# Optimization experiments

Hardware: AMD Instinct MI355X
Metric: run time of the kernel (lower is better)

The kernel has to match this reference:

```python
import jax, jax.numpy as jnp
import numpy as np

T, B, S = 32, 64, 64          # tgt_len, batch, src_len
V, E, H, L = 32000, 512, 1024, 2  # vocab, word_vec, rnn_size, layers


def setup_inputs() -> dict:
    key = jax.random.key(0)
    ks = jax.random.split(key, 16)
    s = 0.02
    emb = jax.random.normal(ks[5], (V, E)) * s
    emb = emb.at[0].set(0.0)  # padding_idx=0 row is zero
    return {
        "input": jax.random.randint(ks[0], (T, B), 0, V),
        "h0": jax.random.normal(ks[1], (L, B, H)) * s,
        "c0": jax.random.normal(ks[2], (L, B, H)) * s,
        "context": jax.random.normal(ks[3], (S, B, H)),
        "init_output": jax.random.normal(ks[4], (B, H)) * s,
        "embedding": emb,
        "W_ih0": jax.random.normal(ks[6], (4 * H, E + H)) * s,  # layer0 input = emb + input-feed
        "W_hh0": jax.random.normal(ks[7], (4 * H, H)) * s,
        "b0": jnp.zeros((4 * H,), jnp.float32),
        "W_ih1": jax.random.normal(ks[8], (4 * H, H)) * s,
        "W_hh1": jax.random.normal(ks[9], (4 * H, H)) * s,
        "b1": jnp.zeros((4 * H,), jnp.float32),
        "attn_in_w": jax.random.normal(ks[10], (H, H)) * s,
        "attn_out_w": jax.random.normal(ks[11], (H, 2 * H)) * s,
        "copy_in_w": jax.random.normal(ks[12], (H, H)) * s,
    }


def _lstm_cell(x, h, c, W_ih, W_hh, b):
    g = x @ W_ih.T + h @ W_hh.T + b
    i, f, gg, o = jnp.split(g, 4, axis=-1)  # PyTorch gate order i,f,g,o
    c_new = jax.nn.sigmoid(f) * c + jax.nn.sigmoid(i) * jnp.tanh(gg)
    h_new = jax.nn.sigmoid(o) * jnp.tanh(c_new)
    return h_new, c_new


def _global_attention(in_w, out_w, query, ctx):
    # query: (B,H), ctx: (B,S,H)
    q = query @ in_w.T
    scores = jnp.einsum('bd,bsd->bs', q, ctx)
    a = jax.nn.softmax(scores, axis=-1)
    wctx = jnp.einsum('bs,bsd->bd', a, ctx)
    out = jnp.tanh(jnp.concatenate([wctx, query], axis=-1) @ out_w.T)
    return out, a


def reference(input, h0, c0, context, init_output, embedding,
              W_ih0, W_hh0, b0, W_ih1, W_hh1, b1,
              attn_in_w, attn_out_w, copy_in_w):
    ctx = jnp.transpose(context, (1, 0, 2))  # (B,S,H)
    emb = embedding[input]                    # (T,B,E)

    def step(carry, emb_t):
        h, c, out_feed = carry
        x = jnp.concatenate([emb_t, out_feed], axis=-1)  # input feed
        h0n, c0n = _lstm_cell(x, h[0], c[0], W_ih0, W_hh0, b0)
        h1n, c1n = _lstm_cell(h0n, h[1], c[1], W_ih1, W_hh1, b1)
        out, a_std = _global_attention(attn_in_w, attn_out_w, h1n, ctx)
        # copy attention: only the weights are kept by the original module
        qc = out @ copy_in_w.T
        a_copy = jax.nn.softmax(jnp.einsum('bd,bsd->bs', qc, ctx), axis=-1)
        new_carry = (jnp.stack([h0n, h1n]), jnp.stack([c0n, c1n]), out)
        return new_carry, (out, a_std, a_copy)

    (h_T, c_T, _), (outputs, attn_std, attn_copy) = jax.lax.scan(
        step, (h0, c0, init_output), emb)
    return outputs, (h_T, c_T), attn_std, attn_copy
```

## Files before the change

kernel.cpp:

```cpp
#include <hip/hip_runtime.h>

typedef unsigned short u16;
typedef unsigned int   u32;
typedef __attribute__((ext_vector_type(8))) __bf16 bfrag;
typedef __attribute__((ext_vector_type(4))) float  f32x4;
typedef __attribute__((ext_vector_type(2))) u32    u32x2;
typedef __attribute__((ext_vector_type(4))) u32    u32x4;

#define DEVI static __device__ __forceinline__

#define ST2SC(p, v)    asm volatile("global_store_short %0, %1, off sc0 sc1"   :: "v"(p), "v"(v) : "memory")
#define ST4SC(p, v)    asm volatile("global_store_dword %0, %1, off sc0 sc1"   :: "v"(p), "v"(v) : "memory")
#define ST8SC(p, v)    asm volatile("global_store_dwordx2 %0, %1, off sc0 sc1" :: "v"(p), "v"(v) : "memory")
#define ST16SC(p, v)   asm volatile("global_store_dwordx4 %0, %1, off sc0 sc1" :: "v"(p), "v"(v) : "memory")
#define VMFLUSH()      asm volatile("s_waitcnt vmcnt(0)" ::: "memory")

constexpr long OUT_OFF = 0;
constexpr long HT_OFF  = 2097152;
constexpr long CT_OFF  = 2228224;
constexpr long AS_OFF  = 2359296;
constexpr long AC_OFF  = 2490368;

constexpr long WAO_O   = 0;
constexpr long CTX_O   = 4194304;
constexpr long OFR_O   = 0;
constexpr long H0R_O   = 4194304;
constexpr long H1R_O   = 8388608;
constexpr long WAI_O   = 12582912;
constexpr long WC_O    = 14680064;
constexpr long CTXW_O  = 16777216;
constexpr long CTXWC_O = 25165824;
constexpr long CTXOT_O = 33554432;
constexpr long EBF_O   = 41943040;
constexpr long OF0_O   = 44040192;
constexpr long H00_O   = 44171264;
constexpr long H10_O   = 44302336;
constexpr long AB_O    = 44433408;
constexpr long BAR_O   = 44957696;

constexpr int W0LDS_O = 0;
constexpr int W1LDS_O = 81920;
constexpr int SCR_O   = 147456;
constexpr int SCR2_O  = 156160;

struct KParams {
  const int* input; const float* h0; const float* c0; const float* context;
  const float* init_output; const float* embedding;
  const float* W_ih0; const float* W_hh0; const float* b0;
  const float* W_ih1; const float* W_hh1; const float* b1;
  const float* attn_in; const float* attn_out; const float* copy_in;
  float* out; char* ws;
};

DEVI float bf2f(u16 u) { u32 x = ((u32)u) << 16; return __builtin_bit_cast(float, x); }
DEVI u16 f2bf(float f) {
  u32 x = __builtin_bit_cast(u32, f);
  u32 r = x + 0x7fffu + ((x >> 16) & 1u);
  return (u16)(r >> 16);
}
DEVI void cvtc_sc(const float* s, char* d) {
  float4 v = *(const float4*)s;
  u32x2 u;
  u[0] = (u32)f2bf(v.x) | ((u32)f2bf(v.y) << 16);
  u[1] = (u32)f2bf(v.z) | ((u32)f2bf(v.w) << 16);
  ST8SC(d, u);
}
DEVI float sigm(float x)  { return 1.f / (1.f + __expf(-x)); }
DEVI float tanh_(float x) { return 1.f - 2.f / (__expf(2.f * x) + 1.f); }
DEVI f32x4 mfma16(bfrag a, bfrag b, f32x4 c) {
  return __builtin_amdgcn_mfma_f32_16x16x32_bf16(a, b, c, 0, 0, 0);
}
DEVI u32 fragoff(int m, int k) {
  return (u32)((((k >> 5) * 4 + (m >> 4)) * 64 + ((k >> 3) & 3) * 16 + (m & 15)) * 16 + (k & 7) * 2);
}
DEVI char* of_slot(char* w, int s) { return w + (s ? OFR_O + (long)(s - 1) * 131072 : OF0_O); }
DEVI char* h0_slot(char* w, int s) { return w + (s ? H0R_O + (long)(s - 1) * 131072 : H00_O); }
DEVI char* h1_slot(char* w, int s) { return w + (s ? H1R_O + (long)(s - 1) * 131072 : H10_O); }

DEVI void pollflags(u32* flags, u32 gen) {
  int t = threadIdx.x;
  for (;;) {
    u32 a = __hip_atomic_load(&flags[t],       __ATOMIC_RELAXED, __HIP_MEMORY_SCOPE_AGENT);
    u32 b = __hip_atomic_load(&flags[64 + t],  __ATOMIC_RELAXED, __HIP_MEMORY_SCOPE_AGENT);
    u32 c = __hip_atomic_load(&flags[128 + t], __ATOMIC_RELAXED, __HIP_MEMORY_SCOPE_AGENT);
    u32 d = __hip_atomic_load(&flags[192 + t], __ATOMIC_RELAXED, __HIP_MEMORY_SCOPE_AGENT);
    if (__all((a >= gen) && (b >= gen) && (c >= gen) && (d >= gen))) break;
    __builtin_amdgcn_s_sleep(1);
  }
}
DEVI void barr_arrive(u32* flags, u32 gen) {
  VMFLUSH();
  __syncthreads();
  if (threadIdx.x == 0)
    __hip_atomic_store(&flags[blockIdx.x], gen, __ATOMIC_RELAXED, __HIP_MEMORY_SCOPE_AGENT);
}
DEVI void barr_wait(u32* flags, u32 gen) {
  if (threadIdx.x < 64) pollflags(flags, gen);
  __syncthreads();
  asm volatile("" ::: "memory");
}

template<int N4>
DEVI void gseg(f32x4& acc, const char* Af, int kkA0, int mt, int lane,
               const char* W, int wRowK, int kkW0, int brow, int ke) {
  const u32 sw = (u32)((brow & 7) << 4);
#pragma unroll
  for (int g = 0; g < N4; ++g) {
#pragma unroll
    for (int q = 0; q < 4; ++q) {
      const char* pa = Af + ((((kkA0 + g * 4 + q) * 4 + mt) * 64 + lane) << 4);
      bfrag av = *(const bfrag*)pa;
      int kkW = kkW0 + g * 4 + q;
      u32 off = ((u32)(brow * wRowK + kkW * 32 + ke) * 2) ^ sw;
      acc = mfma16(av, *(const bfrag*)(W + off), acc);
    }
  }
}

DEVI void scr_store(float* scr, int slot, f32x4 acc) {
  const int lane = threadIdx.x & 63;
#pragma unroll
  for (int r = 0; r < 4; ++r)
    scr[slot * 272 + ((lane >> 4) * 4 + r) * 17 + (lane & 15)] = acc[r];
}

DEVI void pointwise64(int bid, const float* scr, const float* bias, float (&cst)[4], char* hfrag) {
  const int m = threadIdx.x;
  const int mt = m >> 4, ml = m & 15;
  u32 hp0 = 0, hp1 = 0;
#pragma unroll
  for (int u = 0; u < 4; ++u) {
    const int j = bid * 4 + u;
    float g0 = scr[(mt*2)*272 + ml*17 + u]      + scr[(mt*2+1)*272 + ml*17 + u]      + bias[j];
    float g1 = scr[(mt*2)*272 + ml*17 + 4 + u]  + scr[(mt*2+1)*272 + ml*17 + 4 + u]  + bias[1024 + j];
    float g2 = scr[(mt*2)*272 + ml*17 + 8 + u]  + scr[(mt*2+1)*272 + ml*17 + 8 + u]  + bias[2048 + j];
    float g3 = scr[(mt*2)*272 + ml*17 + 12 + u] + scr[(mt*2+1)*272 + ml*17 + 12 + u] + bias[3072 + j];
    float cn = sigm(g1) * cst[u] + sigm(g0) * tanh_(g2);
    cst[u] = cn;
    u32 hb = (u32)f2bf(sigm(g3) * tanh_(cn));
    if (u == 0) hp0 = hb; else if (u == 1) hp0 |= hb << 16;
    else if (u == 2) hp1 = hb; else hp1 |= hb << 16;
  }
  u32x2 v; v[0] = hp0; v[1] = hp1;
  ST8SC(hfrag + fragoff(m, bid * 4), v);
}

DEVI void ctxw_gemm(int mt, const u16* Ctx, const u16* Wm, u16* dst) {
  const int tid = threadIdx.x, lane = tid & 63, w = tid >> 6;
  const int arow = mt * 16 + (lane & 15);
  const int ke = (lane >> 4) * 8;
#pragma unroll
  for (int i = 0; i < 8; ++i) {
    int nt = w * 8 + i;
    const u16* A = Ctx + (long)arow * 1024 + ke;
    const u16* B = Wm + (long)(nt * 16 + (lane & 15)) * 1024 + ke;
    f32x4 acc = {0.f, 0.f, 0.f, 0.f};
    for (int kk = 0; kk < 1024; kk += 32)
      acc = mfma16(*(const bfrag*)(A + kk), *(const bfrag*)(B + kk), acc);
#pragma unroll
    for (int r = 0; r < 4; ++r)
      ST2SC((char*)(dst + (long)(mt * 16 + (lane >> 4) * 4 + r) * 1024 + nt * 16 + (lane & 15)),
            (u32)f2bf(acc[r]));
  }
}

DEVI void ctxo_gemm(int bid, const u16* Ctx, const u16* Wao, u16* dst) {
  const int tid = threadIdx.x, lane = tid & 63, w = tid >> 6;
  const int arow = bid * 16 + (lane & 15);
  const int ke = (lane >> 4) * 8;
  const int b = bid >> 2, s0 = (bid & 3) * 16 + (lane >> 4) * 4;
#pragma unroll
  for (int i = 0; i < 8; ++i) {
    int nt = w * 8 + i;
    int j = nt * 16 + (lane & 15);
    const u16* A = Ctx + (long)arow * 1024 + ke;
    const u16* B = Wao + (long)j * 2048 + ke;
    f32x4 acc = {0.f, 0.f, 0.f, 0.f};
    for (int kk = 0; kk < 1024; kk += 32)
      acc = mfma16(*(const bfrag*)(A + kk), *(const bfrag*)(B + kk), acc);
    u32x2 q;
    q[0] = (u32)f2bf(acc[0]) | ((u32)f2bf(acc[1]) << 16);
    q[1] = (u32)f2bf(acc[2]) | ((u32)f2bf(acc[3]) << 16);
    ST8SC((char*)(dst + ((long)(b * 1024 + j) * 64 + s0)), q);
  }
}

__global__ __launch_bounds__(512, 1) void decoder_kernel(KParams p) {
  extern __shared__ char smem[];
  char*  W0   = smem + W0LDS_O;
  char*  W1   = smem + W1LDS_O;
  float* scr  = (float*)(smem + SCR_O);
  float* scr2 = (float*)(smem + SCR2_O);

  char* wsb = p.ws;
  u16* Wao   = (u16*)(wsb + WAO_O);
  u16* Wai   = (u16*)(wsb + WAI_O);
  u16* Wc    = (u16*)(wsb + WC_O);
  u16* Ctx   = (u16*)(wsb + CTX_O);
  u16* CtxW  = (u16*)(wsb + CTXW_O);
  u16* CtxWc = (u16*)(wsb + CTXWC_O);
  u16* CtxOT = (u16*)(wsb + CTXOT_O);
  u32* bar   = (u32*)(wsb + BAR_O);

  const int bid = blockIdx.x, tid = threadIdx.x;
  const int lane = tid & 63, w = tid >> 6;
  const long gtid = (long)bid * 512 + tid, NT = 256l * 512;
  u32 gen = 1;

  {
    float* tile = (float*)smem;
    for (int pass = 0; pass < 2; ++pass) {
      const float* src = pass ? p.copy_in : p.attn_in;
      u16* dst = pass ? Wc : Wai;
      int tr = bid >> 4, tc = bid & 15;
      {
        int r = tid >> 3, c = (tid & 7) * 8;
        const float4* s4 = (const float4*)(src + (long)(tr * 64 + r) * 1024 + tc * 64 + c);
        float4 a = s4[0], b = s4[1];
        float* tp = tile + r * 69 + c;
        tp[0] = a.x; tp[1] = a.y; tp[2] = a.z; tp[3] = a.w;
        tp[4] = b.x; tp[5] = b.y; tp[6] = b.z; tp[7] = b.w;
      }
      __syncthreads();
      {
        int r2 = tid >> 3, c2 = (tid & 7) * 8;
        u32x4 q;
#pragma unroll
        for (int i = 0; i < 4; ++i) {
          float lo = tile[(c2 + 2 * i) * 69 + r2];
          float hi = tile[(c2 + 2 * i + 1) * 69 + r2];
          q[i] = (u32)f2bf(lo) | ((u32)f2bf(hi) << 16);
        }
        ST16SC((char*)(dst + (long)(tc * 64 + r2) * 1024 + tr * 64 + c2), q);
      }
      __syncthreads();
    }
  }

  for (int i = tid; i < 5120; i += 512) {
    int row = i / 320, k = (i % 320) * 8;
    int R = (row >> 2) * 1024 + bid * 4 + (row & 3);
    const float* src = (k < 1536) ? (p.W_ih0 + (long)R * 1536 + k)
                                  : (p.W_hh0 + (long)R * 1024 + (k - 1536));
    float4 a = *(const float4*)src, b = *(const float4*)(src + 4);
    uint4 q;
    q.x = (u32)f2bf(a.x) | ((u32)f2bf(a.y) << 16);
    q.y = (u32)f2bf(a.z) | ((u32)f2bf(a.w) << 16);
    q.z = (u32)f2bf(b.x) | ((u32)f2bf(b.y) << 16);
    q.w = (u32)f2bf(b.z) | ((u32)f2bf(b.w) << 16);
    u32 off = ((u32)(row * 2560 + k) * 2) ^ ((u32)((row & 7) << 4));
    *(uint4*)(W0 + off) = q;
  }
  for (int i = tid; i < 4096; i += 512) {
    int row = i / 256, k = (i % 256) * 8;
    int R = (row >> 2) * 1024 + bid * 4 + (row & 3);
    const float* src = (k < 1024) ? (p.W_ih1 + (long)R * 1024 + k)
                                  : (p.W_hh1 + (long)R * 1024 + (k - 1024));
    float4 a = *(const float4*)src, b = *(const float4*)(src + 4);
    uint4 q;
    q.x = (u32)f2bf(a.x) | ((u32)f2bf(a.y) << 16);
    q.y = (u32)f2bf(a.z) | ((u32)f2bf(a.w) << 16);
    q.z = (u32)f2bf(b.x) | ((u32)f2bf(b.y) << 16);
    q.w = (u32)f2bf(b.z) | ((u32)f2bf(b.w) << 16);
    u32 off = ((u32)(row * 2048 + k) * 2) ^ ((u32)((row & 7) << 4));
    *(uint4*)(W1 + off) = q;
  }

  for (long i = gtid; i < 524288; i += NT) cvtc_sc(p.attn_out + i * 4, (char*)(Wao + i * 4));
  for (long i = gtid; i < 1048576; i += NT) {
    long b = i >> 14, s = (i >> 8) & 63, kq = i & 255;
    cvtc_sc(p.context + ((s * 64 + b) * 1024 + kq * 4), (char*)(Ctx + i * 4));
  }
  for (long i = gtid; i < 262144; i += NT) {
    long row = i >> 7; long t = row >> 6, b = row & 63;
    long k0 = (i & 127) * 4;
    long tok = p.input[row];
    cvtc_sc(p.embedding + tok * 512 + k0, wsb + EBF_O + t * 65536 + fragoff((int)b, (int)k0));
  }
  for (long i = gtid; i < 16384; i += NT) {
    long b = i >> 8, k0 = (i & 255) * 4;
    cvtc_sc(p.init_output + i * 4, of_slot(wsb, 0) + fragoff((int)b, (int)k0));
  }
  for (long i = gtid; i < 32768; i += NT) {
    long l = i >> 14, rem = i & 16383, b = rem >> 8, k0 = (rem & 255) * 4;
    cvtc_sc(p.h0 + i * 4, (l ? h1_slot(wsb, 0) : h0_slot(wsb, 0)) + fragoff((int)b, (int)k0));
  }

  float cR0[4] = {0.f, 0.f, 0.f, 0.f}, cR1[4] = {0.f, 0.f, 0.f, 0.f};
  if (tid < 64) {
#pragma unroll
    for (int u = 0; u < 4; ++u) {
      cR0[u] = p.c0[(long)tid * 1024 + bid * 4 + u];
      cR1[u] = p.c0[65536 + (long)tid * 1024 + bid * 4 + u];
    }
  }

  barr_arrive(bar, gen); barr_wait(bar, gen); ++gen;

  ctxw_gemm(bid, Ctx, Wai, CtxW);
  ctxw_gemm(bid, Ctx, Wc, CtxWc);
  ctxo_gemm(bid, Ctx, Wao, CtxOT);
  barr_arrive(bar, gen); barr_wait(bar, gen); ++gen;

  const int xcd = bid & 7, idx = bid >> 3;
  const int ntP4 = xcd * 8 + (idx & 7), mtP4 = idx >> 3;
  const int browP4 = ntP4 * 16 + (lane & 15);
  const int ke_ = (lane >> 4) * 8;
  bfrag waoreg[4];
#pragma unroll
  for (int q = 0; q < 4; ++q)
    waoreg[q] = *(const bfrag*)(Wao + (long)browP4 * 2048 + 1024 + (w * 4 + q) * 32 + ke_);

  const int mt_ = w & 3, kh_ = w >> 2;
  const int brow_ = lane & 15;

  f32x4 accP1 = {0.f, 0.f, 0.f, 0.f}, accP2;
  {
    const char* E0  = wsb + EBF_O;
    const char* H0p = h0_slot(wsb, 0);
    if (kh_ == 0) {
      gseg<2>(accP1, E0,  0,  mt_, lane, W0, 2560, 0,  brow_, ke_);
      gseg<4>(accP1, H0p, 0,  mt_, lane, W0, 2560, 48, brow_, ke_);
    } else {
      gseg<2>(accP1, E0,  8,  mt_, lane, W0, 2560, 8,  brow_, ke_);
      gseg<4>(accP1, H0p, 16, mt_, lane, W0, 2560, 64, brow_, ke_);
    }
  }

  for (int t = 0; t < 32; ++t) {
    const char* OFc   = of_slot(wsb, t);
    char*       Hb0cF = h0_slot(wsb, t + 1);
    char*       Hb1cF = h1_slot(wsb, t + 1);
    const char* Hb1pF = h1_slot(wsb, t);
    char*       ABt   = wsb + AB_O + (long)t * 16384;

    {
      f32x4 acc = accP1;
      if (kh_ == 0) gseg<4>(acc, OFc, 0,  mt_, lane, W0, 2560, 16, brow_, ke_);
      else          gseg<4>(acc, OFc, 16, mt_, lane, W0, 2560, 32, brow_, ke_);
      scr_store(scr, mt_ * 2 + kh_, acc);
      __syncthreads();
      if (tid < 64) pointwise64(bid, scr, p.b0, cR0, Hb0cF);
    }
    barr_arrive(bar, gen);
    accP2 = f32x4{0.f, 0.f, 0.f, 0.f};
    if (kh_ == 0) gseg<4>(accP2, Hb1pF, 0,  mt_, lane, W1, 2048, 32, brow_, ke_);
    else          gseg<4>(accP2, Hb1pF, 16, mt_, lane, W1, 2048, 48, brow_, ke_);
    barr_wait(bar, gen); ++gen;

    {
      f32x4 acc = accP2;
      if (kh_ == 0) gseg<4>(acc, Hb0cF, 0,  mt_, lane, W1, 2048, 0,  brow_, ke_);
      else          gseg<4>(acc, Hb0cF, 16, mt_, lane, W1, 2048, 16, brow_, ke_);
      scr_store(scr, mt_ * 2 + kh_, acc);
      __syncthreads();
      if (tid < 64) pointwise64(bid, scr, p.b1, cR1, Hb1cF);
    }
    barr_arrive(bar, gen);
    accP1 = f32x4{0.f, 0.f, 0.f, 0.f};
    {
      const char* En = wsb + EBF_O + (long)((t + 1) & 31) * 65536;
      if (kh_ == 0) {
        gseg<2>(accP1, En,    0,  mt_, lane, W0, 2560, 0,  brow_, ke_);
        gseg<2>(accP1, Hb0cF, 0,  mt_, lane, W0, 2560, 48, brow_, ke_);
      } else {
        gseg<2>(accP1, En,    8,  mt_, lane, W0, 2560, 8,  brow_, ke_);
        gseg<2>(accP1, Hb0cF, 16, mt_, lane, W0, 2560, 64, brow_, ke_);
      }
    }
    barr_wait(bar, gen); ++gen;

    if (bid < 64) {
      const int b = bid;
      float h1v[16];
      {
        int k0 = lane * 16;
        const u32* hp0 = (const u32*)(Hb1cF + fragoff(b, k0));
        const u32* hp1 = (const u32*)(Hb1cF + fragoff(b, k0 + 8));
        u32 uu[8] = {hp0[0], hp0[1], hp0[2], hp0[3], hp1[0], hp1[1], hp1[2], hp1[3]};
#pragma unroll
        for (int i = 0; i < 8; ++i) {
          h1v[2 * i]     = bf2f((u16)(uu[i] & 0xffff));
          h1v[2 * i + 1] = bf2f((u16)(uu[i] >> 16));
        }
      }
      const u16* cwb = CtxW + (long)b * 65536;
#pragma unroll
      for (int si = 0; si < 8; ++si) {
        int s = w * 8 + si;
        const u32* u = (const u32*)(cwb + (long)s * 1024 + lane * 16);
        float acc = 0.f;
#pragma unroll
        for (int i = 0; i < 8; ++i) {
          u32 x = u[i];
          acc += h1v[2 * i] * bf2f((u16)(x & 0xffff));
          acc += h1v[2 * i + 1] * bf2f((u16)(x >> 16));
        }
#pragma unroll
        for (int off = 32; off; off >>= 1) acc += __shfl_down(acc, off, 64);
        if (lane == 0) scr2[s] = acc;
      }
      __syncthreads();
      if (w == 0) {
        float v = scr2[lane];
        float mx = v;
#pragma unroll
        for (int off = 32; off; off >>= 1) mx = fmaxf(mx, __shfl_xor(mx, off, 64));
        float e = __expf(v - mx);
        float sm = e;
#pragma unroll
        for (int off = 32; off; off >>= 1) sm += __shfl_xor(sm, off, 64);
        float a = e / sm;
        ST4SC(ABt + (u32)(b * 64 + lane) * 4, __builtin_bit_cast(u32, a));
        ST4SC((char*)(p.out + AS_OFF + (long)t * 4096 + b * 64 + lane), __builtin_bit_cast(u32, a));
      }
    }
    {
      const char* bp = Hb1cF;
      bfrag h0_ = *(const bfrag*)(bp + ((((w * 4 + 0) * 4 + mtP4) * 64 + lane) << 4));
      bfrag h1_ = *(const bfrag*)(bp + ((((w * 4 + 1) * 4 + mtP4) * 64 + lane) << 4));
      bfrag h2_ = *(const bfrag*)(bp + ((((w * 4 + 2) * 4 + mtP4) * 64 + lane) << 4));
      bfrag h3_ = *(const bfrag*)(bp + ((((w * 4 + 3) * 4 + mtP4) * 64 + lane) << 4));
      f32x4 a4 = {0.f, 0.f, 0.f, 0.f};
      a4 = mfma16(h0_, waoreg[0], a4);
      a4 = mfma16(h1_, waoreg[1], a4);
      a4 = mfma16(h2_, waoreg[2], a4);
      a4 = mfma16(h3_, waoreg[3], a4);
      scr_store(scr, w, a4);
    }
    barr_arrive(bar, gen);
    if (kh_ == 0) gseg<2>(accP1, Hb0cF, 8,  mt_, lane, W0, 2560, 56, brow_, ke_);
    else          gseg<2>(accP1, Hb0cF, 24, mt_, lane, W0, 2560, 72, brow_, ke_);
    barr_wait(bar, gen); ++gen;

    {
      {
        int b0i = tid >> 6, s0i = tid & 63;
        int b1i = (tid + 512) >> 6;
        scr2[tid]       = *(const float*)(ABt + (u32)(((mtP4 * 16 + b0i) * 64 + s0i)) * 4);
        scr2[tid + 512] = *(const float*)(ABt + (u32)(((mtP4 * 16 + b1i) * 64 + s0i)) * 4);
      }
      __syncthreads();
      const int pair = tid >> 1, half = tid & 1;
      const int m_l = pair >> 4, j_l = pair & 15;
      const int b = mtP4 * 16 + m_l, j = ntP4 * 16 + j_l;
      const u32* cp = (const u32*)(CtxOT + ((long)(b * 1024 + j) * 64 + half * 32));
      const float* al = scr2 + m_l * 64 + half * 32;
      float acc = 0.f;
#pragma unroll
      for (int i = 0; i < 16; ++i) {
        u32 x = cp[i];
        acc += al[2 * i] * bf2f((u16)(x & 0xffff));
        acc += al[2 * i + 1] * bf2f((u16)(x >> 16));
      }
      float v = acc + __shfl_xor(acc, 1, 64);
      if (half == 0) {
        float h1p = 0.f;
#pragma unroll
        for (int q = 0; q < 8; ++q) h1p += scr[q * 272 + m_l * 17 + j_l];
        v = tanh_(v + h1p);
        ST4SC((char*)(p.out + (long)t * 65536 + b * 1024 + j), __builtin_bit_cast(u32, v));
        u32 hv = (u32)f2bf(v);
        ST2SC(of_slot(wsb, t + 1) + fragoff(b, j), hv);
      }
    }
    barr_arrive(bar, gen);
    barr_wait(bar, gen); ++gen;
  }

  if (tid < 64) {
#pragma unroll
    for (int u = 0; u < 4; ++u) {
      int j = bid * 4 + u;
      p.out[CT_OFF + (long)tid * 1024 + j]         = cR0[u];
      p.out[CT_OFF + 65536 + (long)tid * 1024 + j] = cR1[u];
    }
  }
  if (tid < 256) {
    int u = tid >> 6, m = tid & 63, j = bid * 4 + u;
    u16 a0 = *(const u16*)(h0_slot(wsb, 32) + fragoff(m, j));
    u16 a1 = *(const u16*)(h1_slot(wsb, 32) + fragoff(m, j));
    p.out[HT_OFF + (long)m * 1024 + j]         = bf2f(a0);
    p.out[HT_OFF + 65536 + (long)m * 1024 + j] = bf2f(a1);
  }

  if (bid < 64) {
    const int b = bid;
    u16* cw = (u16*)smem;
    __syncthreads();
    {
      const uint4* src = (const uint4*)(CtxWc + (long)b * 65536);
      uint4* dst = (uint4*)cw;
      for (int i = tid; i < 8192; i += 512) dst[i] = src[i];
    }
    __syncthreads();
    float* lds_s = scr;
    for (int t = 0; t < 32; ++t) {
      float ov[16];
      {
        const float4* op = (const float4*)(p.out + (long)t * 65536 + b * 1024 + lane * 16);
#pragma unroll
        for (int i = 0; i < 4; ++i) {
          float4 v = op[i];
          ov[4 * i] = v.x; ov[4 * i + 1] = v.y; ov[4 * i + 2] = v.z; ov[4 * i + 3] = v.w;
        }
      }
#pragma unroll
      for (int si = 0; si < 8; ++si) {
        int s = w * 8 + si;
        const u32* u = (const u32*)(cw + s * 1024 + lane * 16);
        float acc = 0.f;
#pragma unroll
        for (int i = 0; i < 8; ++i) {
          u32 x = u[i];
          acc += ov[2 * i] * bf2f((u16)(x & 0xffff));
          acc += ov[2 * i + 1] * bf2f((u16)(x >> 16));
        }
#pragma unroll
        for (int off = 32; off; off >>= 1) acc += __shfl_down(acc, off, 64);
        if (lane == 0) lds_s[s] = acc;
      }
      __syncthreads();
      if (w == 0) {
        float v = lds_s[lane];
        float mx = v;
#pragma unroll
        for (int off = 32; off; off >>= 1) mx = fmaxf(mx, __shfl_xor(mx, off, 64));
        float e = __expf(v - mx);
        float sm = e;
#pragma unroll
        for (int off = 32; off; off >>= 1) sm += __shfl_xor(sm, off, 64);
        p.out[AC_OFF + (long)t * 4096 + b * 64 + lane] = e / sm;
      }
      __syncthreads();
    }
  }
}

extern "C" void kernel_launch(void* const* d_in, const int* in_sizes, int n_in,
                              void* d_out, int out_size, void* d_ws, size_t ws_size,
                              hipStream_t stream) {
  KParams p;
  p.input       = (const int*)d_in[0];
  p.h0          = (const float*)d_in[1];
  p.c0          = (const float*)d_in[2];
  p.context     = (const float*)d_in[3];
  p.init_output = (const float*)d_in[4];
  p.embedding   = (const float*)d_in[5];
  p.W_ih0       = (const float*)d_in[6];
  p.W_hh0       = (const float*)d_in[7];
  p.b0          = (const float*)d_in[8];
  p.W_ih1       = (const float*)d_in[9];
  p.W_hh1       = (const float*)d_in[10];
  p.b1          = (const float*)d_in[11];
  p.attn_in     = (const float*)d_in[12];
  p.attn_out    = (const float*)d_in[13];
  p.copy_in     = (const float*)d_in[14];
  p.out         = (float*)d_out;
  p.ws          = (char*)d_ws;

  (void)hipFuncSetAttribute((const void*)decoder_kernel,
                            hipFuncAttributeMaxDynamicSharedMemorySize, 160256);
  (void)hipMemsetAsync((char*)d_ws + BAR_O, 0, 2048, stream);
  void* args[] = { &p };
  (void)hipLaunchCooperativeKernel((void*)decoder_kernel, dim3(256), dim3(512),
                                   args, 160256, stream);
}
```

Before: 1.679 ms.

## Replace a grid barrier with per-batch attention flags and centralize barrier polling

One full grid barrier per timestep is removed. Blocks that need the attention weights now spin on per-batch-row ready flags, which producer blocks set after flushing their stores. The layer-0 partial GEMM that used to overlap that barrier is moved into the remaining barrier's arrive/wait window. Barrier waiting is also restructured so a single block (block 128) polls all 256 arrival flags and publishes one broadcast word that the other blocks poll. Init barriers use explicit release/acquire fences. The costs are an extra hop in every remaining barrier and a larger memset to zero the flag region.

```diff
diff --git a/kernel.cpp b/kernel.cpp
--- a/kernel.cpp
+++ b/kernel.cpp
@@ -36,7 +36,8 @@
 constexpr long H00_O   = 44171264;
 constexpr long H10_O   = 44302336;
 constexpr long AB_O    = 44433408;
-constexpr long BAR_O   = 44957696;
+constexpr long AFLAG_O = 44957696;
+constexpr long BAR_O   = 44965888;
 
 constexpr int W0LDS_O = 0;
 constexpr int W1LDS_O = 81920;
@@ -95,9 +96,30 @@
     __hip_atomic_store(&flags[blockIdx.x], gen, __ATOMIC_RELAXED, __HIP_MEMORY_SCOPE_AGENT);
 }
 DEVI void barr_wait(u32* flags, u32 gen) {
-  if (threadIdx.x < 64) pollflags(flags, gen);
+  u32* bc = flags + 320;
+  if (blockIdx.x == 128) {
+    if (threadIdx.x < 64) pollflags(flags, gen);
+    __syncthreads();
+    if (threadIdx.x == 0)
+      __hip_atomic_store(bc, gen, __ATOMIC_RELAXED, __HIP_MEMORY_SCOPE_AGENT);
+  } else {
+    if (threadIdx.x == 0) {
+      while (__hip_atomic_load(bc, __ATOMIC_RELAXED, __HIP_MEMORY_SCOPE_AGENT) < gen)
+        __builtin_amdgcn_s_sleep(1);
+    }
+  }
   __syncthreads();
   asm volatile("" ::: "memory");
+}
+DEVI void gsync_fence(u32* flags, u32 gen) {
+  __syncthreads();
+  if (threadIdx.x == 0) {
+    __builtin_amdgcn_fence(__ATOMIC_RELEASE, "agent");
+    __hip_atomic_store(&flags[blockIdx.x], gen, __ATOMIC_RELAXED, __HIP_MEMORY_SCOPE_AGENT);
+  }
+  if (threadIdx.x < 64) pollflags(flags, gen);
+  if (threadIdx.x == 0) __builtin_amdgcn_fence(__ATOMIC_ACQUIRE, "agent");
+  __syncthreads();
 }
 
 template<int N4>
@@ -295,12 +317,12 @@
     }
   }
 
-  barr_arrive(bar, gen); barr_wait(bar, gen); ++gen;
+  gsync_fence(bar, gen); ++gen;
 
   ctxw_gemm(bid, Ctx, Wai, CtxW);
   ctxw_gemm(bid, Ctx, Wc, CtxWc);
   ctxo_gemm(bid, Ctx, Wao, CtxOT);
-  barr_arrive(bar, gen); barr_wait(bar, gen); ++gen;
+  gsync_fence(bar, gen); ++gen;
 
   const int xcd = bid & 7, idx = bid >> 3;
   const int ntP4 = xcd * 8 + (idx & 7), mtP4 = idx >> 3;
@@ -413,6 +435,9 @@
         float a = e / sm;
         ST4SC(ABt + (u32)(b * 64 + lane) * 4, __builtin_bit_cast(u32, a));
         ST4SC((char*)(p.out + AS_OFF + (long)t * 4096 + b * 64 + lane), __builtin_bit_cast(u32, a));
+        VMFLUSH();
+        if (lane == 0)
+          ST4SC(wsb + AFLAG_O + ((u32)t * 64 + b) * 4, 1u);
       }
     }
     {
@@ -428,12 +453,14 @@
       a4 = mfma16(h3_, waoreg[3], a4);
       scr_store(scr, w, a4);
     }
-    barr_arrive(bar, gen);
-    if (kh_ == 0) gseg<2>(accP1, Hb0cF, 8,  mt_, lane, W0, 2560, 56, brow_, ke_);
-    else          gseg<2>(accP1, Hb0cF, 24, mt_, lane, W0, 2560, 72, brow_, ke_);
-    barr_wait(bar, gen); ++gen;
 
     {
+      if (tid < 16) {
+        const u32* fp = (const u32*)(wsb + AFLAG_O + ((u32)t * 64 + mtP4 * 16 + tid) * 4);
+        while (__hip_atomic_load(fp, __ATOMIC_RELAXED, __HIP_MEMORY_SCOPE_AGENT) == 0)
+          __builtin_amdgcn_s_sleep(1);
+      }
+      __syncthreads();
       {
         int b0i = tid >> 6, s0i = tid & 63;
         int b1i = (tid + 512) >> 6;
@@ -465,6 +492,8 @@
       }
     }
     barr_arrive(bar, gen);
+    if (kh_ == 0) gseg<2>(accP1, Hb0cF, 8,  mt_, lane, W0, 2560, 56, brow_, ke_);
+    else          gseg<2>(accP1, Hb0cF, 24, mt_, lane, W0, 2560, 72, brow_, ke_);
     barr_wait(bar, gen); ++gen;
   }
 
@@ -561,7 +590,7 @@
 
   (void)hipFuncSetAttribute((const void*)decoder_kernel,
                             hipFuncAttributeMaxDynamicSharedMemorySize, 160256);
-  (void)hipMemsetAsync((char*)d_ws + BAR_O, 0, 2048, stream);
+  (void)hipMemsetAsync((char*)d_ws + AB_O, 0, 534528, stream);
   void* args[] = { &p };
   (void)hipLaunchCooperativeKernel((void*)decoder_kernel, dim3(256), dim3(512),
                                    args, 160256, stream);
```

New measurement: 1.631 ms. -2.8%, faster.
